# Kernel tuning notes

Measured on AMD Instinct MI355X. Metric: run time of the kernel, lower is better.

Reference implementation:

```python
import jax, jax.numpy as jnp
import numpy as np

# ---- module hyperparameters (match init_kwargs) ----
B = 4            # number of point clouds (equal-sized for jit-friendliness)
NB = 4096        # points per cloud; N = B*NB = 16384
N = B * NB
D_IN = 64        # feature dim of x
RATIO = 0.25
MB = int(RATIO * NB)   # 1024 sampled centroids per cloud
R = 0.2                # ball radius
K = 64                 # max_num_neighbors
MLP = [D_IN + 3, 128, 128, 256]


def setup_inputs() -> dict:
    key = jax.random.key(0)
    ks = jax.random.split(key, 8)
    x = jax.random.normal(ks[0], (N, D_IN), dtype=jnp.float32)
    pos = jax.random.uniform(ks[1], (N, 3), dtype=jnp.float32)  # unit cube
    batch = (jnp.arange(N, dtype=jnp.int32) // NB)              # equal-sized clouds
    def lin(k, fan_in, fan_out):
        w = jax.random.normal(k, (fan_in, fan_out), dtype=jnp.float32) * (1.0 / np.sqrt(fan_in))
        b = jnp.zeros((fan_out,), dtype=jnp.float32)
        return w, b
    W1, b1 = lin(ks[2], MLP[0], MLP[1])
    W2, b2 = lin(ks[3], MLP[1], MLP[2])
    W3, b3 = lin(ks[4], MLP[2], MLP[3])
    return {"x": x, "pos": pos, "batch": batch,
            "W1": W1, "b1": b1, "W2": W2, "b2": b2, "W3": W3, "b3": b3}


def _fps_one(p):
    """Farthest point sampling on one cloud p:[NB,3] -> [MB] indices (start at 0)."""
    def body(k, state):
        sel, dist = state
        last = p[sel[k - 1]]                               # [3]
        d2 = jnp.sum((p - last) ** 2, axis=-1)             # [NB]
        dist = jnp.minimum(dist, d2)
        sel = sel.at[k].set(jnp.argmax(dist).astype(jnp.int32))
        return sel, dist
    sel0 = jnp.zeros((MB,), dtype=jnp.int32)
    dist0 = jnp.full((NB,), jnp.inf, dtype=p.dtype)
    sel, _ = jax.lax.fori_loop(1, MB, body, (sel0, dist0))
    return sel


def _radius_one(p, sel):
    """For each centroid, first K in-ball neighbor indices (by index order, like torch_cluster.radius)."""
    q = p[sel]                                              # [MB,3]
    d2 = jnp.sum((q[:, None, :] - p[None, :, :]) ** 2, -1) # [MB,NB]
    mask = d2 <= R * R
    order_key = jnp.where(mask, jnp.arange(NB, dtype=jnp.int32)[None, :], NB)
    nbr = jnp.argsort(order_key, axis=1)[:, :K]            # [MB,K] first-K in-ball
    valid = jnp.take_along_axis(mask, nbr, axis=1)          # [MB,K]
    return nbr, valid


def _conv_one(p, xb, sel, nbr, valid, W1, b1, W2, b2, W3, b3):
    """PointNetConv: msg = MLP(cat(x_j, pos_j - pos_i)), max-aggregated over the ball."""
    q = p[sel]                                   # [MB,3]
    rel = p[nbr] - q[:, None, :]                 # [MB,K,3]
    feat = jnp.concatenate([xb[nbr], rel], -1)   # [MB,K,67]
    h = jax.nn.relu(jnp.einsum('mki,io->mko', feat, W1) + b1)
    h = jax.nn.relu(jnp.einsum('mki,io->mko', h, W2) + b2)
    h = jax.nn.relu(jnp.einsum('mki,io->mko', h, W3) + b3)
    h = jnp.where(valid[..., None], h, -1e9)
    return jnp.max(h, axis=1)                    # [MB,256]


def reference(x, pos, batch, W1, b1, W2, b2, W3, b3):
    # batch is arange(N)//NB: clouds are contiguous and equal-sized -> reshape.
    pos_b = pos.reshape(B, NB, 3)
    x_b = x.reshape(B, NB, D_IN)
    sel = jax.vmap(_fps_one)(pos_b)                         # [B,MB]
    nbr, valid = jax.vmap(_radius_one)(pos_b, sel)          # [B,MB,K]
    out = jax.vmap(_conv_one, in_axes=(0, 0, 0, 0, 0, None, None, None, None, None, None))(
        pos_b, x_b, sel, nbr, valid, W1, b1, W2, b2, W3, b3)  # [B,MB,256]
    x_out = out.reshape(B * MB, MLP[-1])
    pos_out = jnp.take_along_axis(pos_b, sel[..., None], axis=1).reshape(B * MB, 3)
    batch_out = jnp.repeat(jnp.arange(B, dtype=jnp.int32), MB)
    return x_out, pos_out, batch_out
```

## Files before the change

kernel.cpp:

```cpp
#include <hip/hip_runtime.h>

typedef unsigned int UI;
typedef unsigned long long ULL;
typedef _Float16 f16;
typedef _Float16 h8 __attribute__((ext_vector_type(8)));
typedef float f32x4 __attribute__((ext_vector_type(4)));
typedef float fl2 __attribute__((ext_vector_type(2)));

#define NB_PTS 4096
#define MB_SEL 1024
#define KNBR   64
#define NCLOUD 4
#define NCENT  4096

#define WT2_OFF 12288
#define WT3_OFF 28672
#define WS_ELEMS 61440
#define WSFLAG_MAGIC 0x1234ABCDu

#define OFF_H1   13312
#define OFF_H2   30720
#define OFF_PMAX 48128
#define OFF_MASK 49152
#define OFF_NBR  49664
#define OFF_NV   49920
#define OFF_SHS  49924
#define OFF_SLOT 65536
#define DYN_LDS  86016

__device__ __forceinline__ double d2_np64(double dx, double dy, double dz) {
  return __dadd_rn(__dadd_rn(__dmul_rn(dx, dx), __dmul_rn(dy, dy)),
                   __dmul_rn(dz, dz));
}


template <int CTRL>
__device__ __forceinline__ double dpp_fmax_step(double cur) {
  ULL cu = __builtin_bit_cast(ULL, cur);
  UI lo = (UI)cu, hi = (UI)(cu >> 32);
  UI nl = (UI)__builtin_amdgcn_update_dpp(0, (int)lo, CTRL, 0xf, 0xf, true);
  UI nh = (UI)__builtin_amdgcn_update_dpp(0, (int)hi, CTRL, 0xf, 0xf, true);
  double nv = __builtin_bit_cast(double, ((ULL)nh << 32) | (ULL)nl);
  return fmax(cur, nv);
}

__global__ __launch_bounds__(512, 2) void fused_kernel(
    const float* __restrict__ x, const float* __restrict__ pos,
    const float* __restrict__ W1, const float* __restrict__ b1,
    const float* __restrict__ W2, const float* __restrict__ b2,
    const float* __restrict__ W3, const float* __restrict__ b3,
    f16* __restrict__ ws, UI* __restrict__ wsflag,
    float* __restrict__ selstash, float* __restrict__ out_x,
    float* __restrict__ out_pos, float* __restrict__ out_batch) {
  extern __shared__ char smem[];
  const int tid  = threadIdx.x;
  const int lane = tid & 63;
  const int wv   = tid >> 6;

  if (blockIdx.x == NCLOUD) {
    for (int t = tid; t < WS_ELEMS; t += 512) {
      if (t < WT2_OFF) {
        int n = t / 96, k = t - n * 96;
        ws[t] = (k < 67) ? (f16)W1[k * 128 + n] : (f16)0.f;
      } else if (t < WT3_OFF) {
        int u = t - WT2_OFF;
        int n = u >> 7, k = u & 127;
        ws[t] = (f16)W2[k * 128 + n];
      } else {
        int u = t - WT3_OFF;
        int n = u >> 7, k = u & 127;
        ws[t] = (f16)W3[k * 256 + n];
      }
    }
    __syncthreads();
    if (tid == 0)
      __hip_atomic_store(wsflag, WSFLAG_MAGIC, __ATOMIC_RELEASE,
                         __HIP_MEMORY_SCOPE_AGENT);
    return;
  }

  if (blockIdx.x < NCLOUD) {
#pragma clang fp contract(off)
    asm volatile("s_setprio 3");
    float4* pp = (float4*)smem;
    ULL* slots = (ULL*)(smem + OFF_SLOT);
    const int b = blockIdx.x;

    fl2 mx[4], my[4], mz[4], dist[4];
#pragma unroll
    for (int t = 0; t < 4; ++t) {
      int j0 = tid + (2 * t) * 512;
      int j1 = tid + (2 * t + 1) * 512;
      size_t a0 = ((size_t)b * NB_PTS + j0) * 3;
      size_t a1 = ((size_t)b * NB_PTS + j1) * 3;
      float X0 = pos[a0], Y0 = pos[a0 + 1], Z0 = pos[a0 + 2];
      float X1 = pos[a1], Y1 = pos[a1 + 1], Z1 = pos[a1 + 2];
      pp[j0] = make_float4(X0, Y0, Z0, 0.f);
      pp[j1] = make_float4(X1, Y1, Z1, 0.f);
      mx[t] = fl2{X0, X1}; my[t] = fl2{Y0, Y1}; mz[t] = fl2{Z0, Z1};
      dist[t] = fl2{__builtin_inff(), __builtin_inff()};
    }
    if (tid == 0)
      __hip_atomic_store(&selstash[b * MB_SEL], 1.0f, __ATOMIC_RELAXED,
                         __HIP_MEMORY_SCOPE_AGENT);
    __syncthreads();

    int cur = 0;
    for (int k = 1; k < MB_SEL; ++k) {
      float4 w = pp[cur];
      float bestv = -__builtin_inff();
      int   besti = 0x7fffffff;
#pragma unroll
      for (int t = 0; t < 4; ++t) {
        fl2 dx = mx[t] - w.x;
        fl2 dy = my[t] - w.y;
        fl2 dz = mz[t] - w.z;
        fl2 dd = (dx * dx + dy * dy) + dz * dz;
        fl2 dc = dist[t];
        float d0 = fminf(dc.x, dd.x);
        float d1 = fminf(dc.y, dd.y);
        dist[t] = fl2{d0, d1};
        if (d0 > bestv) { bestv = d0; besti = tid + (2 * t) * 512; }
        if (d1 > bestv) { bestv = d1; besti = tid + (2 * t + 1) * 512; }
      }
      double key = __builtin_bit_cast(
          double, ((ULL)__float_as_uint(bestv) << 32) | (ULL)(~(UI)besti));
      key = dpp_fmax_step<0x111>(key);
      key = dpp_fmax_step<0x112>(key);
      key = dpp_fmax_step<0x114>(key);
      key = dpp_fmax_step<0x118>(key);
      key = dpp_fmax_step<0x142>(key);
      key = dpp_fmax_step<0x143>(key);
      const int buf = (k & 1) * 8;
      if (lane == 63) slots[buf + wv] = __builtin_bit_cast(ULL, key);
      asm volatile("s_waitcnt lgkmcnt(0)\n\ts_barrier" ::: "memory");
      const double* sp = (const double*)(slots + buf);
      double s0 = sp[0], s1 = sp[1], s2 = sp[2], s3 = sp[3];
      double s4 = sp[4], s5 = sp[5], s6 = sp[6], s7 = sp[7];
      double m01 = fmax(s0, s1);
      double m23 = fmax(s2, s3);
      double m45 = fmax(s4, s5);
      double m67 = fmax(s6, s7);
      double mk  = fmax(fmax(m01, m23), fmax(m45, m67));
      int winner = (int)(~(UI)__builtin_bit_cast(ULL, mk));
      if (tid == 0)
        __hip_atomic_store(&selstash[b * MB_SEL + k], (float)(winner + 1),
                           __ATOMIC_RELAXED, __HIP_MEMORY_SCOPE_AGENT);
      cur = winner;
    }
    return;
  }

  f16* featA  = (f16*)smem;
  f16* h1s    = (f16*)(smem + OFF_H1);
  f16* h2s    = (f16*)(smem + OFF_H2);
  float* pmax = (float*)(smem + OFF_PMAX);
  ULL* masks  = (ULL*)(smem + OFF_MASK);
  int* nbrS   = (int*)(smem + OFF_NBR);
  int* nvP    = (int*)(smem + OFF_NV);
  int* shS    = (int*)(smem + OFF_SHS);

  const int c  = (int)blockIdx.x - (NCLOUD + 1);
  const int k  = c >> 2;
  const int b  = c & 3;
  const int cg = b * MB_SEL + k;

  if (tid == 0) {
    while (__hip_atomic_load(wsflag, __ATOMIC_ACQUIRE,
                             __HIP_MEMORY_SCOPE_AGENT) != WSFLAG_MAGIC)
      __builtin_amdgcn_s_sleep(2);
  }
  __syncthreads();

  const int n    = lane & 15;
  const int quad = lane >> 4;
  const int col  = wv * 16 + n;
  h8 B1f[3], B2f[4];
  float bv1, bv2, bv3[2];
  bv1 = b1[col];
  bv2 = b2[col];
#pragma unroll
  for (int kt = 0; kt < 3; ++kt)
    B1f[kt] = *(const h8*)(ws + col * 96 + kt * 32 + quad * 8);
#pragma unroll
  for (int kt = 0; kt < 4; ++kt)
    B2f[kt] = *(const h8*)(ws + WT2_OFF + col * 128 + kt * 32 + quad * 8);
#pragma unroll
  for (int ct = 0; ct < 2; ++ct) bv3[ct] = b3[(2 * wv + ct) * 16 + n];

  if (tid == 0) {
    float v;
    for (;;) {
      v = __hip_atomic_load(&selstash[cg], __ATOMIC_RELAXED,
                            __HIP_MEMORY_SCOPE_AGENT);
      if (v >= 1.0f) break;
      __builtin_amdgcn_s_sleep(8);
    }
    *shS = (int)v - 1;
  }
  __syncthreads();
  const int s = (*shS) & (NB_PTS - 1);

  const size_t qb = ((size_t)(b * NB_PTS + s)) * 3;
  const float qxf = pos[qb], qyf = pos[qb + 1], qzf = pos[qb + 2];
  const double qx = (double)qxf, qy = (double)qyf, qz = (double)qzf;
  const double RR = 0.2 * 0.2;

#pragma unroll
  for (int it = 0; it < 8; ++it) {
    const int ch = wv * 8 + it;
    const int j  = ch * 64 + lane;
    const size_t pb = ((size_t)b * NB_PTS + j) * 3;
    double d2 = d2_np64((double)pos[pb] - qx, (double)pos[pb + 1] - qy,
                        (double)pos[pb + 2] - qz);
    ULL m = __ballot(d2 <= RR);
    if (lane == 0) masks[ch] = m;
  }
  __syncthreads();

  if (tid < 64) {
    ULL m = masks[tid];
    int pc = __popcll(m);
    int incl = pc;
#pragma unroll
    for (int off = 1; off < 64; off <<= 1) {
      int o = __shfl_up(incl, off, 64);
      if (tid >= off) incl += o;
    }
    int base = incl - pc;
    int tot  = __shfl(incl, 63, 64);
    int nvw  = min(tot, KNBR);
    if (tid == 63) *nvP = nvw;
    int slot = base;
    ULL mm = m;
    while (mm && slot < KNBR) {
      int bit = __ffsll(mm) - 1;
      nbrS[slot++] = tid * 64 + bit;
      mm &= mm - 1;
    }
    if (tid >= nvw) nbrS[tid] = s;
  }
  __syncthreads();
  const int nv = *nvP;

  {
    const int r = tid >> 3;
    const int part = tid & 7;
    const int g = nbrS[r];
    const float* xrow = x + (((size_t)(b * NB_PTS + g)) << 6) + part * 8;
    float4 u0 = *(const float4*)(xrow);
    float4 u1 = *(const float4*)(xrow + 4);
    h8 o0;
    o0[0]=(f16)u0.x; o0[1]=(f16)u0.y; o0[2]=(f16)u0.z; o0[3]=(f16)u0.w;
    o0[4]=(f16)u1.x; o0[5]=(f16)u1.y; o0[6]=(f16)u1.z; o0[7]=(f16)u1.w;
    *(h8*)(featA + r * 104 + part * 8) = o0;
    if (part == 7) {
      size_t gb = ((size_t)(b * NB_PTS + g)) * 3;
      h8 rv = {(f16)0.f,(f16)0.f,(f16)0.f,(f16)0.f,(f16)0.f,(f16)0.f,(f16)0.f,(f16)0.f};
      rv[0] = (f16)(pos[gb]     - qxf);
      rv[1] = (f16)(pos[gb + 1] - qyf);
      rv[2] = (f16)(pos[gb + 2] - qzf);
      h8 z = {(f16)0.f,(f16)0.f,(f16)0.f,(f16)0.f,(f16)0.f,(f16)0.f,(f16)0.f,(f16)0.f};
      *(h8*)(featA + r * 104 + 64) = rv;
      *(h8*)(featA + r * 104 + 72) = z;
      *(h8*)(featA + r * 104 + 80) = z;
      *(h8*)(featA + r * 104 + 88) = z;
    }
  }
  __syncthreads();

#pragma unroll
  for (int at = 0; at < 4; ++at) {
    f32x4 acc = {0.f, 0.f, 0.f, 0.f};
#pragma unroll
    for (int kt = 0; kt < 3; ++kt) {
      h8 a = *(const h8*)(featA + (at * 16 + n) * 104 + kt * 32 + quad * 8);
      acc = __builtin_amdgcn_mfma_f32_16x16x32_f16(a, B1f[kt], acc, 0, 0, 0);
    }
#pragma unroll
    for (int r = 0; r < 4; ++r)
      h1s[(at * 16 + quad * 4 + r) * 136 + col] = (f16)fmaxf(acc[r] + bv1, 0.f);
  }
  __syncthreads();

#pragma unroll
  for (int at = 0; at < 4; ++at) {
    f32x4 acc = {0.f, 0.f, 0.f, 0.f};
#pragma unroll
    for (int kt = 0; kt < 4; ++kt) {
      h8 a = *(const h8*)(h1s + (at * 16 + n) * 136 + kt * 32 + quad * 8);
      acc = __builtin_amdgcn_mfma_f32_16x16x32_f16(a, B2f[kt], acc, 0, 0, 0);
    }
#pragma unroll
    for (int r = 0; r < 4; ++r)
      h2s[(at * 16 + quad * 4 + r) * 136 + col] = (f16)fmaxf(acc[r] + bv2, 0.f);
  }
  __syncthreads();

  float vm[2] = {0.f, 0.f};
#pragma unroll
  for (int at = 0; at < 4; ++at) {
#pragma unroll
    for (int ct = 0; ct < 2; ++ct) {
      const int c3 = (2 * wv + ct) * 16 + n;
      f32x4 acc = {0.f, 0.f, 0.f, 0.f};
#pragma unroll
      for (int kt = 0; kt < 4; ++kt) {
        h8 a = *(const h8*)(h2s + (at * 16 + n) * 136 + kt * 32 + quad * 8);
        h8 wfr = *(const h8*)(ws + WT3_OFF + c3 * 128 + kt * 32 + quad * 8);
        acc = __builtin_amdgcn_mfma_f32_16x16x32_f16(a, wfr, acc, 0, 0, 0);
      }
#pragma unroll
      for (int r = 0; r < 4; ++r) {
        float h = fmaxf(acc[r] + bv3[ct], 0.f);
        const int row = at * 16 + quad * 4 + r;
        vm[ct] = fmaxf(vm[ct], row < nv ? h : 0.f);
      }
    }
  }
#pragma unroll
  for (int ct = 0; ct < 2; ++ct) {
    vm[ct] = fmaxf(vm[ct], __shfl_xor(vm[ct], 16, 64));
    vm[ct] = fmaxf(vm[ct], __shfl_xor(vm[ct], 32, 64));
  }
  if (quad == 0) {
#pragma unroll
    for (int ct = 0; ct < 2; ++ct) pmax[(2 * wv + ct) * 16 + n] = vm[ct];
  }
  __syncthreads();

  if (tid < 256) out_x[(size_t)cg * 256 + tid] = pmax[tid];
  if (tid < 3) out_pos[cg * 3 + tid] = pos[qb + tid];
  if (tid == 0) out_batch[cg] = (float)b;
}

extern "C" void kernel_launch(void* const* d_in, const int* in_sizes, int n_in,
                              void* d_out, int out_size, void* d_ws, size_t ws_size,
                              hipStream_t stream) {
  const float* x   = (const float*)d_in[0];
  const float* pos = (const float*)d_in[1];
  const float* W1 = (const float*)d_in[3];
  const float* b1 = (const float*)d_in[4];
  const float* W2 = (const float*)d_in[5];
  const float* b2 = (const float*)d_in[6];
  const float* W3 = (const float*)d_in[7];
  const float* b3 = (const float*)d_in[8];

  float* out = (float*)d_out;
  float* out_pos   = out + (size_t)NCENT * 256;
  float* out_batch = out_pos + (size_t)NCENT * 3;
  f16* ws    = (f16*)d_ws;
  UI* wsflag = (UI*)((char*)d_ws + 2 * WS_ELEMS);

  hipFuncSetAttribute((const void*)fused_kernel,
                      hipFuncAttributeMaxDynamicSharedMemorySize, DYN_LDS);

  fused_kernel<<<NCLOUD + 1 + NCENT, 512, DYN_LDS, stream>>>(
      x, pos, W1, b1, W2, b2, W3, b3, ws, wsflag,
      out_batch, out, out_pos, out_batch);
}
```

Measured before the change: 657.5 us.

## Replace FPS per-iteration barrier with LDS ring spin-wait

The farthest-point-sampling loop no longer uses a workgroup barrier each iteration to combine per-wave argmax keys. Each wave publishes its key into a 128-entry ring in shared memory, clears a slot 64 iterations ahead, and spins on atomic loads until all 8 keys for the current iteration are nonzero. The aim is to remove barrier stalls on this serial critical path. In exchange it adds busy polling of shared memory, needs more shared-memory space for the ring, and risks a race on the ring's initial zeroing.

```diff
diff --git a/kernel.cpp b/kernel.cpp
--- a/kernel.cpp
+++ b/kernel.cpp
@@ -83,8 +83,11 @@
 #pragma clang fp contract(off)
     asm volatile("s_setprio 3");
     float4* pp = (float4*)smem;
-    ULL* slots = (ULL*)(smem + OFF_SLOT);
+    ULL* ring  = (ULL*)(smem + OFF_SLOT);
     const int b = blockIdx.x;
+
+    ring[tid] = 0ULL;
+    ring[tid + 512] = 0ULL;
 
     fl2 mx[4], my[4], mz[4], dist[4];
 #pragma unroll
@@ -131,12 +134,43 @@
       key = dpp_fmax_step<0x118>(key);
       key = dpp_fmax_step<0x142>(key);
       key = dpp_fmax_step<0x143>(key);
-      const int buf = (k & 1) * 8;
-      if (lane == 63) slots[buf + wv] = __builtin_bit_cast(ULL, key);
-      asm volatile("s_waitcnt lgkmcnt(0)\n\ts_barrier" ::: "memory");
-      const double* sp = (const double*)(slots + buf);
-      double s0 = sp[0], s1 = sp[1], s2 = sp[2], s3 = sp[3];
-      double s4 = sp[4], s5 = sp[5], s6 = sp[6], s7 = sp[7];
+      ULL* rb = ring + ((k & 127) << 3);
+      if (lane == 63) {
+        __hip_atomic_store(&rb[wv], __builtin_bit_cast(ULL, key),
+                           __ATOMIC_RELAXED, __HIP_MEMORY_SCOPE_WORKGROUP);
+        __hip_atomic_store(&ring[(((k + 64) & 127) << 3) + wv], 0ULL,
+                           __ATOMIC_RELAXED, __HIP_MEMORY_SCOPE_WORKGROUP);
+      }
+      ULL u0, u1, u2, u3, u4, u5, u6, u7;
+      for (;;) {
+        u0 = __hip_atomic_load(&rb[0], __ATOMIC_RELAXED,
+                               __HIP_MEMORY_SCOPE_WORKGROUP);
+        u1 = __hip_atomic_load(&rb[1], __ATOMIC_RELAXED,
+                               __HIP_MEMORY_SCOPE_WORKGROUP);
+        u2 = __hip_atomic_load(&rb[2], __ATOMIC_RELAXED,
+                               __HIP_MEMORY_SCOPE_WORKGROUP);
+        u3 = __hip_atomic_load(&rb[3], __ATOMIC_RELAXED,
+                               __HIP_MEMORY_SCOPE_WORKGROUP);
+        u4 = __hip_atomic_load(&rb[4], __ATOMIC_RELAXED,
+                               __HIP_MEMORY_SCOPE_WORKGROUP);
+        u5 = __hip_atomic_load(&rb[5], __ATOMIC_RELAXED,
+                               __HIP_MEMORY_SCOPE_WORKGROUP);
+        u6 = __hip_atomic_load(&rb[6], __ATOMIC_RELAXED,
+                               __HIP_MEMORY_SCOPE_WORKGROUP);
+        u7 = __hip_atomic_load(&rb[7], __ATOMIC_RELAXED,
+                               __HIP_MEMORY_SCOPE_WORKGROUP);
+        UI lo = (UI)u0 & (UI)u1 & (UI)u2 & (UI)u3 &
+                (UI)u4 & (UI)u5 & (UI)u6 & (UI)u7;
+        if (lo != 0u) break;
+      }
+      double s0 = __builtin_bit_cast(double, u0);
+      double s1 = __builtin_bit_cast(double, u1);
+      double s2 = __builtin_bit_cast(double, u2);
+      double s3 = __builtin_bit_cast(double, u3);
+      double s4 = __builtin_bit_cast(double, u4);
+      double s5 = __builtin_bit_cast(double, u5);
+      double s6 = __builtin_bit_cast(double, u6);
+      double s7 = __builtin_bit_cast(double, u7);
       double m01 = fmax(s0, s1);
       double m23 = fmax(s2, s3);
       double m45 = fmax(s4, s5);
```

Result: slower. 713.1 us (+8.5%).
